# Performance work log

Hardware: AMD Instinct MI355X
Metric: run time of the kernel (lower is better)

The kernel has to match this reference:

```python
import jax, jax.numpy as jnp
import numpy as np

N_NODES = 100000
N_EDGES = 1600000
IN_CH = 128
HID = 128
OUT_CH = 2
NUM_GRAPHS = 512


def _mlp_params(key, d_in, d_out):
    k1, k2 = jax.random.split(key)
    s1 = 1.0 / np.sqrt(d_in)
    s2 = 1.0 / np.sqrt(d_out)
    return (jax.random.uniform(k1, (d_in, d_out), jnp.float32, -s1, s1),
            jnp.zeros((d_out,), jnp.float32),
            jax.random.uniform(k2, (d_out, d_out), jnp.float32, -s2, s2),
            jnp.zeros((d_out,), jnp.float32))


def setup_inputs() -> dict:
    key = jax.random.key(0)
    ks = jax.random.split(key, 8)
    x = jax.random.normal(ks[0], (N_NODES, IN_CH), jnp.float32)
    edge_index = jax.random.randint(ks[1], (2, N_EDGES), 0, N_NODES, jnp.int64)
    batch = jnp.sort(jax.random.randint(ks[2], (N_NODES,), 0, NUM_GRAPHS, jnp.int64))
    w1_0, b1_0, w2_0, b2_0 = _mlp_params(ks[3], IN_CH, HID)
    w1_1, b1_1, w2_1, b2_1 = _mlp_params(ks[4], HID, HID)
    w1_2, b1_2, w2_2, b2_2 = _mlp_params(ks[5], HID, HID)
    s = 1.0 / np.sqrt(HID)
    w_lin = jax.random.uniform(ks[6], (HID, OUT_CH), jnp.float32, -s, s)
    b_lin = jnp.zeros((OUT_CH,), jnp.float32)
    return {"x": x, "edge_index": edge_index, "batch": batch,
            "w1_0": w1_0, "b1_0": b1_0, "w2_0": w2_0, "b2_0": b2_0,
            "w1_1": w1_1, "b1_1": b1_1, "w2_1": w2_1, "b2_1": b2_1,
            "w1_2": w1_2, "b1_2": b1_2, "w2_2": w2_2, "b2_2": b2_2,
            "w_lin": w_lin, "b_lin": b_lin}


def _gin_conv(x, src, dst, w1, b1, w2, b2):
    # GINConv with eps=0: MLP(x + sum_{j in N(i)} x_j)
    agg = jax.ops.segment_sum(x[src], dst, num_segments=N_NODES)  # [N, d]
    h = x + agg
    h = jax.nn.relu(h @ w1 + b1)
    return h @ w2 + b2


def reference(x, edge_index, batch,
              w1_0, b1_0, w2_0, b2_0,
              w1_1, b1_1, w2_1, b2_1,
              w1_2, b1_2, w2_2, b2_2,
              w_lin, b_lin):
    src, dst = edge_index[0], edge_index[1]
    h = _gin_conv(x, src, dst, w1_0, b1_0, w2_0, b2_0)
    h = jax.nn.relu(h)
    h = jax.nn.relu(_gin_conv(h, src, dst, w1_1, b1_1, w2_1, b2_1))
    h = jax.nn.relu(h)  # forward applies relu twice after GIN1
    h = _gin_conv(h, src, dst, w1_2, b1_2, w2_2, b2_2)
    # global mean pool per graph
    sums = jax.ops.segment_sum(h, batch, num_segments=NUM_GRAPHS)  # [G, d]
    counts = jax.ops.segment_sum(jnp.ones((N_NODES,), h.dtype), batch,
                                 num_segments=NUM_GRAPHS)
    pooled = sums / jnp.maximum(counts, 1.0)[:, None]
    # dropout is identity in eval mode
    return pooled @ w_lin + b_lin  # [G, OUT_CH]
```

## Files before the change

### kernel.cpp

```cpp
#include <hip/hip_runtime.h>
#include <hip/hip_bf16.h>

#define N_NODES   100000
#define N_EDGES   1600000
#define IN_CH     128
#define HID       128
#define OUT_CH    2
#define NUM_GRAPHS 512

#define BKT_SHIFT 9
#define NB2 ((N_NODES + 511) >> BKT_SHIFT)
#define PB  200
#define CHUNK (N_EDGES / PB)

typedef __attribute__((ext_vector_type(8))) short bf16x8;
typedef __attribute__((ext_vector_type(4))) float f32x4;
typedef unsigned int uint32;
typedef unsigned long long uint64;

static __device__ __forceinline__ float b2f(uint32 b) {
    return __uint_as_float(b << 16);
}
static __device__ __forceinline__ unsigned short f2b(float f) {
    uint32 u = __float_as_uint(f);
    u += 0x7fffu + ((u >> 16) & 1u);
    return (unsigned short)(u >> 16);
}
static __device__ __forceinline__ void acc8(float* a, int4 v) {
    uint32 x;
    x = (uint32)v.x; a[0] += __uint_as_float(x << 16); a[1] += __uint_as_float(x & 0xffff0000u);
    x = (uint32)v.y; a[2] += __uint_as_float(x << 16); a[3] += __uint_as_float(x & 0xffff0000u);
    x = (uint32)v.z; a[4] += __uint_as_float(x << 16); a[5] += __uint_as_float(x & 0xffff0000u);
    x = (uint32)v.w; a[6] += __uint_as_float(x << 16); a[7] += __uint_as_float(x & 0xffff0000u);
}

__global__ void k_cast(const float* __restrict__ x, unsigned short* __restrict__ h) {
    int i = blockIdx.x * blockDim.x + threadIdx.x;
    int base = i * 4;
    float4 v = *(const float4*)(x + base);
    ushort4 o;
    o.x = f2b(v.x); o.y = f2b(v.y); o.z = f2b(v.z); o.w = f2b(v.w);
    *(ushort4*)(h + base) = o;
}

__global__ void k_wprep(const float* w0, const float* w1, const float* w2,
                        const float* w3, const float* w4, const float* w5,
                        unsigned short* __restrict__ wt) {
    const float* ws[6] = {w0, w1, w2, w3, w4, w5};
    const float* w = ws[blockIdx.x];
    unsigned short* o = wt + blockIdx.x * 16384;
    for (int i = threadIdx.x; i < 16384; i += 256) {
        int k = i >> 7, n = i & 127;
        o[n * 128 + k] = f2b(w[i]);
    }
}

__global__ void k_p1(const int* __restrict__ dst, int* __restrict__ histG) {
    __shared__ int h[NB2];
    int t = threadIdx.x, blk = blockIdx.x;
    for (int i = t; i < NB2; i += 512) h[i] = 0;
    __syncthreads();
    int base = blk * CHUNK;
    for (int i = t; i < CHUNK; i += 512)
        atomicAdd(&h[dst[base + i] >> BKT_SHIFT], 1);
    __syncthreads();
    for (int i = t; i < NB2; i += 512) histG[i * PB + blk] = h[i];
}

__global__ void k_scan1(const int* __restrict__ in, int* __restrict__ out,
                        int* __restrict__ bsum, int n) {
    __shared__ int sm[256];
    int b = blockIdx.x, t = threadIdx.x;
    int base = b * 1024 + t * 4;
    int v0 = 0, v1 = 0, v2 = 0, v3 = 0;
    if (base + 3 < n) {
        int4 q = *(const int4*)(in + base);
        v0 = q.x; v1 = q.y; v2 = q.z; v3 = q.w;
    } else {
        if (base + 0 < n) v0 = in[base + 0];
        if (base + 1 < n) v1 = in[base + 1];
        if (base + 2 < n) v2 = in[base + 2];
        if (base + 3 < n) v3 = in[base + 3];
    }
    int s = v0 + v1 + v2 + v3;
    sm[t] = s;
    __syncthreads();
    for (int off = 1; off < 256; off <<= 1) {
        int u = (t >= off) ? sm[t - off] : 0;
        __syncthreads();
        sm[t] += u;
        __syncthreads();
    }
    int p = (t == 0) ? 0 : sm[t - 1];
    int o0 = p, o1 = p + v0, o2 = o1 + v1, o3 = o2 + v2;
    if (base + 3 < n) {
        *(int4*)(out + base) = make_int4(o0, o1, o2, o3);
    } else {
        if (base + 0 < n) out[base + 0] = o0;
        if (base + 1 < n) out[base + 1] = o1;
        if (base + 2 < n) out[base + 2] = o2;
        if (base + 3 < n) out[base + 3] = o3;
    }
    if (t == 255) bsum[b] = s + ((t == 0) ? 0 : sm[t - 1]);
}

__global__ void k_scan2(int* __restrict__ bsum, int nb) {
    __shared__ int sm[128];
    int t = threadIdx.x;
    int v = (t < nb) ? bsum[t] : 0;
    sm[t] = v;
    __syncthreads();
    for (int off = 1; off < 128; off <<= 1) {
        int u = (t >= off) ? sm[t - off] : 0;
        __syncthreads();
        sm[t] += u;
        __syncthreads();
    }
    int p = (t == 0) ? 0 : sm[t - 1];
    if (t < nb) bsum[t] = p;
}

__global__ void k_scan3b(int* __restrict__ out, const int* __restrict__ bsum, int n) {
    int b = blockIdx.x, t = threadIdx.x;
    int base = b * 1024 + t * 4;
    int add = bsum[b];
    if (base + 3 < n) {
        int4 q = *(const int4*)(out + base);
        q.x += add; q.y += add; q.z += add; q.w += add;
        *(int4*)(out + base) = q;
    } else {
        for (int j = 0; j < 4; ++j)
            if (base + j < n) out[base + j] += add;
    }
}

__global__ void k_p3(const int* __restrict__ ei, const int* __restrict__ baseG,
                     uint64* __restrict__ ebuf) {
    __shared__ int cur[NB2];
    int t = threadIdx.x, blk = blockIdx.x;
    for (int i = t; i < NB2; i += 512) cur[i] = baseG[i * PB + blk];
    __syncthreads();
    int base = blk * CHUNK;
    for (int i = t; i < CHUNK; i += 512) {
        int e = base + i;
        int src = ei[e];
        int dst = ei[N_EDGES + e];
        int pos = atomicAdd(&cur[dst >> BKT_SHIFT], 1);
        ebuf[pos] = ((uint64)(uint32)dst << 32) | (uint32)src;
    }
}

__global__ void k_p4(const uint64* __restrict__ ebuf, const int* __restrict__ baseG,
                     int* __restrict__ off, int* __restrict__ csr) {
    __shared__ int ldeg[512];
    __shared__ int lscan[512];
    __shared__ int lcur[512];
    int b = blockIdx.x, t = threadIdx.x;
    int node0 = b << BKT_SHIFT;
    int nn = min(512, N_NODES - node0);
    int e0 = baseG[b * PB];
    int e1 = (b == NB2 - 1) ? N_EDGES : baseG[(b + 1) * PB];
    ldeg[t] = 0;
    __syncthreads();
    for (int e = e0 + t; e < e1; e += 512) {
        int dst = (int)(ebuf[e] >> 32);
        atomicAdd(&ldeg[dst - node0], 1);
    }
    __syncthreads();
    lscan[t] = ldeg[t];
    __syncthreads();
    for (int o = 1; o < 512; o <<= 1) {
        int v = (t >= o) ? lscan[t - o] : 0;
        __syncthreads();
        lscan[t] += v;
        __syncthreads();
    }
    int excl = (t == 0) ? 0 : lscan[t - 1];
    lcur[t] = e0 + excl;
    if (t < nn) off[node0 + t] = e0 + excl;
    if (b == NB2 - 1 && t == 0) off[N_NODES] = N_EDGES;
    __syncthreads();
    for (int e = e0 + t; e < e1; e += 512) {
        uint64 pr = ebuf[e];
        int dst = (int)(pr >> 32);
        int pos = atomicAdd(&lcur[dst - node0], 1);
        csr[pos] = (int)(pr & 0xffffffffu);
    }
}

__global__ void k_goff(const int* __restrict__ batch, int* __restrict__ goff) {
    int g = blockIdx.x * blockDim.x + threadIdx.x;
    if (g > NUM_GRAPHS) return;
    int lo = 0, hi = N_NODES;
    while (lo < hi) {
        int mid = (lo + hi) >> 1;
        if (batch[mid] < g) lo = mid + 1; else hi = mid;
    }
    goff[g] = lo;
}

__global__ void k_agg(const unsigned short* __restrict__ h,
                      const int* __restrict__ off, const int* __restrict__ csr,
                      unsigned short* __restrict__ hs) {
    int wid = (blockIdx.x * 256 + threadIdx.x) >> 6;
    int lane = threadIdx.x & 63;
    if (wid >= N_NODES) return;
    int g = lane >> 4, sub = lane & 15;
    int e0 = off[wid], e1 = off[wid + 1];
    float a[8] = {0.f, 0.f, 0.f, 0.f, 0.f, 0.f, 0.f, 0.f};
    int e = e0 + g;
    for (; e + 4 < e1; e += 8) {
        int s0 = csr[e];
        int s1 = csr[e + 4];
        int4 v0 = *(const int4*)(h + (size_t)s0 * 128 + sub * 8);
        int4 v1 = *(const int4*)(h + (size_t)s1 * 128 + sub * 8);
        acc8(a, v0);
        acc8(a, v1);
    }
    if (e < e1) {
        int s0 = csr[e];
        int4 v0 = *(const int4*)(h + (size_t)s0 * 128 + sub * 8);
        acc8(a, v0);
    }
#pragma unroll
    for (int j = 0; j < 8; ++j) {
        a[j] += __shfl_xor(a[j], 16);
        a[j] += __shfl_xor(a[j], 32);
    }
    if (g == 0) {
        int4 sv = *(const int4*)(h + (size_t)wid * 128 + sub * 8);
        acc8(a, sv);
        int4 o;
        o.x = (int)((uint32)f2b(a[0]) | ((uint32)f2b(a[1]) << 16));
        o.y = (int)((uint32)f2b(a[2]) | ((uint32)f2b(a[3]) << 16));
        o.z = (int)((uint32)f2b(a[4]) | ((uint32)f2b(a[5]) << 16));
        o.w = (int)((uint32)f2b(a[6]) | ((uint32)f2b(a[7]) << 16));
        *(int4*)(hs + (size_t)wid * 128 + sub * 8) = o;
    }
}

template<int OUTER_RELU>
__global__ void k_mlp(const unsigned short* __restrict__ hs,
                      const unsigned short* __restrict__ w1t, const float* __restrict__ b1,
                      const unsigned short* __restrict__ w2t, const float* __restrict__ b2,
                      unsigned short* __restrict__ ho) {
    __shared__ unsigned short T[128 * 128];
    int tid = threadIdx.x;
    int lane = tid & 63, wave = tid >> 6;
    int l15 = lane & 15, l4 = lane >> 4;
    int row0 = blockIdx.x * 128;
    int wn0 = wave * 32;

    bf16x8 w1f[2][4], w2f[2][4];
#pragma unroll
    for (int nt = 0; nt < 2; ++nt)
#pragma unroll
        for (int k = 0; k < 4; ++k) {
            int o = (wn0 + nt * 16 + l15) * 128 + k * 32 + l4 * 8;
            w1f[nt][k] = *(const bf16x8*)(w1t + o);
            w2f[nt][k] = *(const bf16x8*)(w2t + o);
        }
    float bias1[2] = { b1[wn0 + l15], b1[wn0 + 16 + l15] };
    float bias2[2] = { b2[wn0 + l15], b2[wn0 + 16 + l15] };

#pragma unroll
    for (int mt = 0; mt < 8; ++mt) {
        int arow = row0 + mt * 16 + l15;
        if (arow >= N_NODES) arow = N_NODES - 1;
        const unsigned short* ap = hs + (size_t)arow * 128 + l4 * 8;
        bf16x8 a0 = *(const bf16x8*)(ap);
        bf16x8 a1 = *(const bf16x8*)(ap + 32);
        bf16x8 a2 = *(const bf16x8*)(ap + 64);
        bf16x8 a3 = *(const bf16x8*)(ap + 96);
#pragma unroll
        for (int nt = 0; nt < 2; ++nt) {
            f32x4 acc = {0.f, 0.f, 0.f, 0.f};
            acc = __builtin_amdgcn_mfma_f32_16x16x32_bf16(a0, w1f[nt][0], acc, 0, 0, 0);
            acc = __builtin_amdgcn_mfma_f32_16x16x32_bf16(a1, w1f[nt][1], acc, 0, 0, 0);
            acc = __builtin_amdgcn_mfma_f32_16x16x32_bf16(a2, w1f[nt][2], acc, 0, 0, 0);
            acc = __builtin_amdgcn_mfma_f32_16x16x32_bf16(a3, w1f[nt][3], acc, 0, 0, 0);
#pragma unroll
            for (int j = 0; j < 4; ++j) {
                float v = fmaxf(acc[j] + bias1[nt], 0.f);
                int trow = mt * 16 + l4 * 4 + j;
                int tcol = wn0 + nt * 16 + l15;
                int byte = (trow * 256 + tcol * 2) ^ ((trow & 7) << 4);
                *(unsigned short*)((char*)T + byte) = f2b(v);
            }
        }
    }
    __syncthreads();

#pragma unroll
    for (int mt = 0; mt < 8; ++mt) {
        int trow = mt * 16 + l15;
        int sw = (trow & 7) << 4;
        int rb = trow * 256 + l4 * 16;
        bf16x8 t0 = *(const bf16x8*)((const char*)T + ((rb + 0)   ^ sw));
        bf16x8 t1 = *(const bf16x8*)((const char*)T + ((rb + 64)  ^ sw));
        bf16x8 t2 = *(const bf16x8*)((const char*)T + ((rb + 128) ^ sw));
        bf16x8 t3 = *(const bf16x8*)((const char*)T + ((rb + 192) ^ sw));
        __syncthreads();
#pragma unroll
        for (int nt = 0; nt < 2; ++nt) {
            f32x4 acc = {0.f, 0.f, 0.f, 0.f};
            acc = __builtin_amdgcn_mfma_f32_16x16x32_bf16(t0, w2f[nt][0], acc, 0, 0, 0);
            acc = __builtin_amdgcn_mfma_f32_16x16x32_bf16(t1, w2f[nt][1], acc, 0, 0, 0);
            acc = __builtin_amdgcn_mfma_f32_16x16x32_bf16(t2, w2f[nt][2], acc, 0, 0, 0);
            acc = __builtin_amdgcn_mfma_f32_16x16x32_bf16(t3, w2f[nt][3], acc, 0, 0, 0);
#pragma unroll
            for (int j = 0; j < 4; ++j) {
                float v = acc[j] + bias2[nt];
                if (OUTER_RELU) v = fmaxf(v, 0.f);
                int orow = mt * 16 + l4 * 4 + j;
                int ocol = wn0 + nt * 16 + l15;
                int byte = (orow * 256 + ocol * 2) ^ ((orow & 7) << 4);
                *(unsigned short*)((char*)T + byte) = f2b(v);
            }
        }
    }
    __syncthreads();

    for (int c = tid; c < 2048; c += 256) {
        int r = c >> 4, cc = c & 15;
        int byte = (r * 256 + cc * 16) ^ ((r & 7) << 4);
        int4 v = *(const int4*)((const char*)T + byte);
        int gr = row0 + r;
        if (gr < N_NODES)
            *(int4*)(ho + (size_t)gr * 128 + cc * 8) = v;
    }
}

__global__ void k_pool(const unsigned short* __restrict__ h,
                       const int* __restrict__ goff,
                       const float* __restrict__ wl, const float* __restrict__ bl,
                       float* __restrict__ out) {
    int g = blockIdx.x;
    int lane = threadIdx.x;
    int e0 = goff[g], e1 = goff[g + 1];
    int c2 = lane << 1;
    float s0 = 0.f, s1 = 0.f;
    int r = e0;
    for (; r + 1 < e1; r += 2) {
        uint32 v0 = *(const uint32*)(h + (size_t)r * 128 + c2);
        uint32 v1 = *(const uint32*)(h + (size_t)(r + 1) * 128 + c2);
        s0 += b2f(v0 & 0xffffu) + b2f(v1 & 0xffffu);
        s1 += b2f(v0 >> 16) + b2f(v1 >> 16);
    }
    if (r < e1) {
        uint32 v = *(const uint32*)(h + (size_t)r * 128 + c2);
        s0 += b2f(v & 0xffffu);
        s1 += b2f(v >> 16);
    }
    float inv = 1.f / fmaxf((float)(e1 - e0), 1.f);
    s0 *= inv; s1 *= inv;
    float o0 = s0 * wl[c2 * 2]     + s1 * wl[(c2 + 1) * 2];
    float o1 = s0 * wl[c2 * 2 + 1] + s1 * wl[(c2 + 1) * 2 + 1];
#pragma unroll
    for (int d = 32; d; d >>= 1) {
        o0 += __shfl_down(o0, d);
        o1 += __shfl_down(o1, d);
    }
    if (lane == 0) {
        out[g * 2]     = o0 + bl[0];
        out[g * 2 + 1] = o1 + bl[1];
    }
}

extern "C" void kernel_launch(void* const* d_in, const int* in_sizes, int n_in,
                              void* d_out, int out_size, void* d_ws, size_t ws_size,
                              hipStream_t stream) {
    const float* x     = (const float*)d_in[0];
    const int*   ei    = (const int*)d_in[1];
    const int*   batch = (const int*)d_in[2];
    const float* w1[3] = {(const float*)d_in[3],  (const float*)d_in[7],  (const float*)d_in[11]};
    const float* b1[3] = {(const float*)d_in[4],  (const float*)d_in[8],  (const float*)d_in[12]};
    const float* w2[3] = {(const float*)d_in[5],  (const float*)d_in[9],  (const float*)d_in[13]};
    const float* b2[3] = {(const float*)d_in[6],  (const float*)d_in[10], (const float*)d_in[14]};
    const float* wl    = (const float*)d_in[15];
    const float* bl    = (const float*)d_in[16];

    char* p = (char*)d_ws;
    auto alloc = [&](size_t bytes) {
        char* r = p;
        p += (bytes + 255) & ~(size_t)255;
        return r;
    };
    int* off    = (int*)alloc((size_t)(N_NODES + 1) * 4);
    int* goff   = (int*)alloc((size_t)(NUM_GRAPHS + 1) * 4);
    int* histG  = (int*)alloc((size_t)(NB2 * PB) * 4);
    int* baseG  = (int*)alloc((size_t)(NB2 * PB + 1) * 4);
    int* bsum   = (int*)alloc((size_t)128 * 4);
    int* csr    = (int*)alloc((size_t)N_EDGES * 4);
    unsigned short* wts = (unsigned short*)alloc((size_t)6 * 16384 * 2);
    unsigned short* hA  = (unsigned short*)alloc((size_t)N_NODES * 128 * 2);
    unsigned short* hS  = (unsigned short*)alloc((size_t)N_NODES * 128 * 2);
    unsigned short* hB  = (unsigned short*)alloc((size_t)N_NODES * 128 * 2);
    uint64* ebuf = (uint64*)hS;

    k_cast<<<(N_NODES * IN_CH / 4 + 255) / 256, 256, 0, stream>>>(x, hA);
    k_wprep<<<6, 256, 0, stream>>>(w1[0], w2[0], w1[1], w2[1], w1[2], w2[2], wts);

    k_p1<<<PB, 512, 0, stream>>>(ei + N_EDGES, histG);
    const int SCAN_N = NB2 * PB;
    const int SCAN_BLOCKS = (SCAN_N + 1023) / 1024;
    k_scan1<<<SCAN_BLOCKS, 256, 0, stream>>>(histG, baseG, bsum, SCAN_N);
    k_scan2<<<1, 128, 0, stream>>>(bsum, SCAN_BLOCKS);
    k_scan3b<<<SCAN_BLOCKS, 256, 0, stream>>>(baseG, bsum, SCAN_N);
    k_p3<<<PB, 512, 0, stream>>>(ei, baseG, ebuf);
    k_p4<<<NB2, 512, 0, stream>>>(ebuf, baseG, off, csr);

    k_goff<<<3, 256, 0, stream>>>(batch, goff);

    unsigned short* wt1[3] = {wts,             wts + 2 * 16384, wts + 4 * 16384};
    unsigned short* wt2[3] = {wts + 1 * 16384, wts + 3 * 16384, wts + 5 * 16384};

    const int AGG_GRID = N_NODES / 4;
    const int MLP_GRID = (N_NODES + 127) / 128;

    k_agg<<<AGG_GRID, 256, 0, stream>>>(hA, off, csr, hS);
    k_mlp<1><<<MLP_GRID, 256, 0, stream>>>(hS, wt1[0], b1[0], wt2[0], b2[0], hB);
    k_agg<<<AGG_GRID, 256, 0, stream>>>(hB, off, csr, hS);
    k_mlp<1><<<MLP_GRID, 256, 0, stream>>>(hS, wt1[1], b1[1], wt2[1], b2[1], hA);
    k_agg<<<AGG_GRID, 256, 0, stream>>>(hA, off, csr, hS);
    k_mlp<0><<<MLP_GRID, 256, 0, stream>>>(hS, wt1[2], b1[2], wt2[2], b2[2], hB);

    k_pool<<<NUM_GRAPHS, 64, 0, stream>>>(hB, goff, wl, bl, (float*)d_out);
}
```

Baseline: 398.1 us.

## Fuse neighbor aggregation into GIN MLP kernel via shared-memory staging

Merges the gather-sum aggregation kernel into the MLP kernel. Each 128-node block aggregates its neighbors into swizzled LDS, then runs both MFMA layers from there, which removes the global write and re-read of the aggregated intermediate and two launches per layer. It also unrolls the edge loop to four loads per iteration. In exchange, each wave processes 32 nodes one after another and the grid is cut from 25000 to 782 blocks, so gather parallelism and memory-latency hiding may fall sharply. A barrier is also moved into the first MFMA loop.

```diff
diff --git a/kernel.cpp b/kernel.cpp
--- a/kernel.cpp
+++ b/kernel.cpp
@@ -199,48 +199,9 @@
     goff[g] = lo;
 }
 
-__global__ void k_agg(const unsigned short* __restrict__ h,
+template<int OUTER_RELU>
+__global__ void k_gin(const unsigned short* __restrict__ h,
                       const int* __restrict__ off, const int* __restrict__ csr,
-                      unsigned short* __restrict__ hs) {
-    int wid = (blockIdx.x * 256 + threadIdx.x) >> 6;
-    int lane = threadIdx.x & 63;
-    if (wid >= N_NODES) return;
-    int g = lane >> 4, sub = lane & 15;
-    int e0 = off[wid], e1 = off[wid + 1];
-    float a[8] = {0.f, 0.f, 0.f, 0.f, 0.f, 0.f, 0.f, 0.f};
-    int e = e0 + g;
-    for (; e + 4 < e1; e += 8) {
-        int s0 = csr[e];
-        int s1 = csr[e + 4];
-        int4 v0 = *(const int4*)(h + (size_t)s0 * 128 + sub * 8);
-        int4 v1 = *(const int4*)(h + (size_t)s1 * 128 + sub * 8);
-        acc8(a, v0);
-        acc8(a, v1);
-    }
-    if (e < e1) {
-        int s0 = csr[e];
-        int4 v0 = *(const int4*)(h + (size_t)s0 * 128 + sub * 8);
-        acc8(a, v0);
-    }
-#pragma unroll
-    for (int j = 0; j < 8; ++j) {
-        a[j] += __shfl_xor(a[j], 16);
-        a[j] += __shfl_xor(a[j], 32);
-    }
-    if (g == 0) {
-        int4 sv = *(const int4*)(h + (size_t)wid * 128 + sub * 8);
-        acc8(a, sv);
-        int4 o;
-        o.x = (int)((uint32)f2b(a[0]) | ((uint32)f2b(a[1]) << 16));
-        o.y = (int)((uint32)f2b(a[2]) | ((uint32)f2b(a[3]) << 16));
-        o.z = (int)((uint32)f2b(a[4]) | ((uint32)f2b(a[5]) << 16));
-        o.w = (int)((uint32)f2b(a[6]) | ((uint32)f2b(a[7]) << 16));
-        *(int4*)(hs + (size_t)wid * 128 + sub * 8) = o;
-    }
-}
-
-template<int OUTER_RELU>
-__global__ void k_mlp(const unsigned short* __restrict__ hs,
                       const unsigned short* __restrict__ w1t, const float* __restrict__ b1,
                       const unsigned short* __restrict__ w2t, const float* __restrict__ b2,
                       unsigned short* __restrict__ ho) {
@@ -249,8 +210,53 @@
     int lane = tid & 63, wave = tid >> 6;
     int l15 = lane & 15, l4 = lane >> 4;
     int row0 = blockIdx.x * 128;
+
+    int g = l4, sub = l15;
+    for (int r = wave * 32; r < wave * 32 + 32; ++r) {
+        int node = row0 + r;
+        if (node >= N_NODES) node = N_NODES - 1;
+        int e0 = off[node], e1 = off[node + 1];
+        float a[8] = {0.f, 0.f, 0.f, 0.f, 0.f, 0.f, 0.f, 0.f};
+        int e = e0 + g;
+        for (; e + 12 < e1; e += 16) {
+            int s0 = csr[e], s1 = csr[e + 4], s2 = csr[e + 8], s3 = csr[e + 12];
+            int4 v0 = *(const int4*)(h + (size_t)s0 * 128 + sub * 8);
+            int4 v1 = *(const int4*)(h + (size_t)s1 * 128 + sub * 8);
+            int4 v2 = *(const int4*)(h + (size_t)s2 * 128 + sub * 8);
+            int4 v3 = *(const int4*)(h + (size_t)s3 * 128 + sub * 8);
+            acc8(a, v0); acc8(a, v1); acc8(a, v2); acc8(a, v3);
+        }
+        for (; e + 4 < e1; e += 8) {
+            int s0 = csr[e], s1 = csr[e + 4];
+            int4 v0 = *(const int4*)(h + (size_t)s0 * 128 + sub * 8);
+            int4 v1 = *(const int4*)(h + (size_t)s1 * 128 + sub * 8);
+            acc8(a, v0); acc8(a, v1);
+        }
+        if (e < e1) {
+            int s0 = csr[e];
+            int4 v0 = *(const int4*)(h + (size_t)s0 * 128 + sub * 8);
+            acc8(a, v0);
+        }
+#pragma unroll
+        for (int j = 0; j < 8; ++j) {
+            a[j] += __shfl_xor(a[j], 16);
+            a[j] += __shfl_xor(a[j], 32);
+        }
+        if (g == 0) {
+            int4 sv = *(const int4*)(h + (size_t)node * 128 + sub * 8);
+            acc8(a, sv);
+            int4 o;
+            o.x = (int)((uint32)f2b(a[0]) | ((uint32)f2b(a[1]) << 16));
+            o.y = (int)((uint32)f2b(a[2]) | ((uint32)f2b(a[3]) << 16));
+            o.z = (int)((uint32)f2b(a[4]) | ((uint32)f2b(a[5]) << 16));
+            o.w = (int)((uint32)f2b(a[6]) | ((uint32)f2b(a[7]) << 16));
+            int byte = (r * 256 + sub * 16) ^ ((r & 7) << 4);
+            *(int4*)((char*)T + byte) = o;
+        }
+    }
+    __syncthreads();
+
     int wn0 = wave * 32;
-
     bf16x8 w1f[2][4], w2f[2][4];
 #pragma unroll
     for (int nt = 0; nt < 2; ++nt)
@@ -265,13 +271,14 @@
 
 #pragma unroll
     for (int mt = 0; mt < 8; ++mt) {
-        int arow = row0 + mt * 16 + l15;
-        if (arow >= N_NODES) arow = N_NODES - 1;
-        const unsigned short* ap = hs + (size_t)arow * 128 + l4 * 8;
-        bf16x8 a0 = *(const bf16x8*)(ap);
-        bf16x8 a1 = *(const bf16x8*)(ap + 32);
-        bf16x8 a2 = *(const bf16x8*)(ap + 64);
-        bf16x8 a3 = *(const bf16x8*)(ap + 96);
+        int trow = mt * 16 + l15;
+        int sw = (trow & 7) << 4;
+        int rb = trow * 256 + l4 * 16;
+        bf16x8 a0 = *(const bf16x8*)((const char*)T + ((rb + 0)   ^ sw));
+        bf16x8 a1 = *(const bf16x8*)((const char*)T + ((rb + 64)  ^ sw));
+        bf16x8 a2 = *(const bf16x8*)((const char*)T + ((rb + 128) ^ sw));
+        bf16x8 a3 = *(const bf16x8*)((const char*)T + ((rb + 192) ^ sw));
+        __syncthreads();
 #pragma unroll
         for (int nt = 0; nt < 2; ++nt) {
             f32x4 acc = {0.f, 0.f, 0.f, 0.f};
@@ -282,14 +289,13 @@
 #pragma unroll
             for (int j = 0; j < 4; ++j) {
                 float v = fmaxf(acc[j] + bias1[nt], 0.f);
-                int trow = mt * 16 + l4 * 4 + j;
-                int tcol = wn0 + nt * 16 + l15;
-                int byte = (trow * 256 + tcol * 2) ^ ((trow & 7) << 4);
+                int orow = mt * 16 + l4 * 4 + j;
+                int ocol = wn0 + nt * 16 + l15;
+                int byte = (orow * 256 + ocol * 2) ^ ((orow & 7) << 4);
                 *(unsigned short*)((char*)T + byte) = f2b(v);
             }
         }
     }
-    __syncthreads();
 
 #pragma unroll
     for (int mt = 0; mt < 8; ++mt) {
@@ -392,11 +398,10 @@
     int* baseG  = (int*)alloc((size_t)(NB2 * PB + 1) * 4);
     int* bsum   = (int*)alloc((size_t)128 * 4);
     int* csr    = (int*)alloc((size_t)N_EDGES * 4);
+    uint64* ebuf = (uint64*)alloc((size_t)N_EDGES * 8);
     unsigned short* wts = (unsigned short*)alloc((size_t)6 * 16384 * 2);
     unsigned short* hA  = (unsigned short*)alloc((size_t)N_NODES * 128 * 2);
-    unsigned short* hS  = (unsigned short*)alloc((size_t)N_NODES * 128 * 2);
     unsigned short* hB  = (unsigned short*)alloc((size_t)N_NODES * 128 * 2);
-    uint64* ebuf = (uint64*)hS;
 
     k_cast<<<(N_NODES * IN_CH / 4 + 255) / 256, 256, 0, stream>>>(x, hA);
     k_wprep<<<6, 256, 0, stream>>>(w1[0], w2[0], w1[1], w2[1], w1[2], w2[2], wts);
@@ -415,15 +420,11 @@
     unsigned short* wt1[3] = {wts,             wts + 2 * 16384, wts + 4 * 16384};
     unsigned short* wt2[3] = {wts + 1 * 16384, wts + 3 * 16384, wts + 5 * 16384};
 
-    const int AGG_GRID = N_NODES / 4;
-    const int MLP_GRID = (N_NODES + 127) / 128;
-
-    k_agg<<<AGG_GRID, 256, 0, stream>>>(hA, off, csr, hS);
-    k_mlp<1><<<MLP_GRID, 256, 0, stream>>>(hS, wt1[0], b1[0], wt2[0], b2[0], hB);
-    k_agg<<<AGG_GRID, 256, 0, stream>>>(hB, off, csr, hS);
-    k_mlp<1><<<MLP_GRID, 256, 0, stream>>>(hS, wt1[1], b1[1], wt2[1], b2[1], hA);
-    k_agg<<<AGG_GRID, 256, 0, stream>>>(hA, off, csr, hS);
-    k_mlp<0><<<MLP_GRID, 256, 0, stream>>>(hS, wt1[2], b1[2], wt2[2], b2[2], hB);
+    const int GIN_GRID = (N_NODES + 127) / 128;
+
+    k_gin<1><<<GIN_GRID, 256, 0, stream>>>(hA, off, csr, wt1[0], b1[0], wt2[0], b2[0], hB);
+    k_gin<1><<<GIN_GRID, 256, 0, stream>>>(hB, off, csr, wt1[1], b1[1], wt2[1], b2[1], hA);
+    k_gin<0><<<GIN_GRID, 256, 0, stream>>>(hA, off, csr, wt1[2], b1[2], wt2[2], b2[2], hB);
 
     k_pool<<<NUM_GRAPHS, 64, 0, stream>>>(hB, goff, wl, bl, (float*)d_out);
 }
```

Result: slower. 468.0 us (+17.6%).

## Restructure MLP to per-wave 16-row tiles and unroll aggregation gather by four

Applied to the files above, without the earlier changes.

The MLP kernel now gives each wave its own 16-row tile in a private 4 KB LDS slab instead of 128 rows per block shared across waves. Weight fragments are loaded from global/L2 per output tile rather than kept in registers, and all block-level barriers are gone. This cuts LDS use and sync overhead and raises occupancy, at the cost of re-reading weights once per 16 rows. Separately, the aggregation loop gets a 4-edge unrolled body per lane group so more gather loads are in flight.

```diff
diff --git a/kernel.cpp b/kernel.cpp
--- a/kernel.cpp
+++ b/kernel.cpp
@@ -32,6 +32,9 @@
     x = (uint32)v.y; a[2] += __uint_as_float(x << 16); a[3] += __uint_as_float(x & 0xffff0000u);
     x = (uint32)v.z; a[4] += __uint_as_float(x << 16); a[5] += __uint_as_float(x & 0xffff0000u);
     x = (uint32)v.w; a[6] += __uint_as_float(x << 16); a[7] += __uint_as_float(x & 0xffff0000u);
+}
+static __device__ __forceinline__ int rswz(int r) {
+    return (((r >> 2) ^ r) & 3) << 5;
 }
 
 __global__ void k_cast(const float* __restrict__ x, unsigned short* __restrict__ h) {
@@ -209,6 +212,14 @@
     int e0 = off[wid], e1 = off[wid + 1];
     float a[8] = {0.f, 0.f, 0.f, 0.f, 0.f, 0.f, 0.f, 0.f};
     int e = e0 + g;
+    for (; e + 12 < e1; e += 16) {
+        int s0 = csr[e], s1 = csr[e + 4], s2 = csr[e + 8], s3 = csr[e + 12];
+        int4 v0 = *(const int4*)(h + (size_t)s0 * 128 + sub * 8);
+        int4 v1 = *(const int4*)(h + (size_t)s1 * 128 + sub * 8);
+        int4 v2 = *(const int4*)(h + (size_t)s2 * 128 + sub * 8);
+        int4 v3 = *(const int4*)(h + (size_t)s3 * 128 + sub * 8);
+        acc8(a, v0); acc8(a, v1); acc8(a, v2); acc8(a, v3);
+    }
     for (; e + 4 < e1; e += 8) {
         int s0 = csr[e];
         int s1 = csr[e + 4];
@@ -244,90 +255,89 @@
                       const unsigned short* __restrict__ w1t, const float* __restrict__ b1,
                       const unsigned short* __restrict__ w2t, const float* __restrict__ b2,
                       unsigned short* __restrict__ ho) {
-    __shared__ unsigned short T[128 * 128];
+    __shared__ char S[4][4096];
     int tid = threadIdx.x;
     int lane = tid & 63, wave = tid >> 6;
+    int w16 = blockIdx.x * 4 + wave;
+    if (w16 >= (N_NODES >> 4)) return;
+    char* Sw = S[wave];
     int l15 = lane & 15, l4 = lane >> 4;
-    int row0 = blockIdx.x * 128;
-    int wn0 = wave * 32;
-
-    bf16x8 w1f[2][4], w2f[2][4];
-#pragma unroll
-    for (int nt = 0; nt < 2; ++nt)
-#pragma unroll
-        for (int k = 0; k < 4; ++k) {
-            int o = (wn0 + nt * 16 + l15) * 128 + k * 32 + l4 * 8;
-            w1f[nt][k] = *(const bf16x8*)(w1t + o);
-            w2f[nt][k] = *(const bf16x8*)(w2t + o);
+    size_t rowbase = (size_t)w16 * 16 * 128;
+    int bo = l15 * 16;
+
+#pragma unroll
+    for (int i = 0; i < 4; ++i) {
+        int r = i * 4 + l4;
+        int4 v = *(const int4*)((const char*)(hs + rowbase) + r * 256 + bo);
+        *(int4*)(Sw + ((r * 256 + bo) ^ rswz(r))) = v;
+    }
+
+    float bias1[8], bias2[8];
+#pragma unroll
+    for (int nt = 0; nt < 8; ++nt) {
+        bias1[nt] = b1[nt * 16 + l15];
+        bias2[nt] = b2[nt * 16 + l15];
+    }
+
+    int frsw = rswz(l15);
+    bf16x8 af[4];
+#pragma unroll
+    for (int k = 0; k < 4; ++k)
+        af[k] = *(const bf16x8*)(Sw + ((l15 * 256 + k * 64 + l4 * 16) ^ frsw));
+
+#pragma unroll
+    for (int nt = 0; nt < 8; ++nt) {
+        const unsigned short* wp = w1t + (nt * 16 + l15) * 128 + l4 * 8;
+        bf16x8 wf0 = *(const bf16x8*)(wp);
+        bf16x8 wf1 = *(const bf16x8*)(wp + 32);
+        bf16x8 wf2 = *(const bf16x8*)(wp + 64);
+        bf16x8 wf3 = *(const bf16x8*)(wp + 96);
+        f32x4 acc = {0.f, 0.f, 0.f, 0.f};
+        acc = __builtin_amdgcn_mfma_f32_16x16x32_bf16(af[0], wf0, acc, 0, 0, 0);
+        acc = __builtin_amdgcn_mfma_f32_16x16x32_bf16(af[1], wf1, acc, 0, 0, 0);
+        acc = __builtin_amdgcn_mfma_f32_16x16x32_bf16(af[2], wf2, acc, 0, 0, 0);
+        acc = __builtin_amdgcn_mfma_f32_16x16x32_bf16(af[3], wf3, acc, 0, 0, 0);
+#pragma unroll
+        for (int j = 0; j < 4; ++j) {
+            float v = fmaxf(acc[j] + bias1[nt], 0.f);
+            int r = l4 * 4 + j;
+            int cb = (nt * 16 + l15) * 2;
+            *(unsigned short*)(Sw + ((r * 256 + cb) ^ rswz(r))) = f2b(v);
         }
-    float bias1[2] = { b1[wn0 + l15], b1[wn0 + 16 + l15] };
-    float bias2[2] = { b2[wn0 + l15], b2[wn0 + 16 + l15] };
-
-#pragma unroll
-    for (int mt = 0; mt < 8; ++mt) {
-        int arow = row0 + mt * 16 + l15;
-        if (arow >= N_NODES) arow = N_NODES - 1;
-        const unsigned short* ap = hs + (size_t)arow * 128 + l4 * 8;
-        bf16x8 a0 = *(const bf16x8*)(ap);
-        bf16x8 a1 = *(const bf16x8*)(ap + 32);
-        bf16x8 a2 = *(const bf16x8*)(ap + 64);
-        bf16x8 a3 = *(const bf16x8*)(ap + 96);
-#pragma unroll
-        for (int nt = 0; nt < 2; ++nt) {
-            f32x4 acc = {0.f, 0.f, 0.f, 0.f};
-            acc = __builtin_amdgcn_mfma_f32_16x16x32_bf16(a0, w1f[nt][0], acc, 0, 0, 0);
-            acc = __builtin_amdgcn_mfma_f32_16x16x32_bf16(a1, w1f[nt][1], acc, 0, 0, 0);
-            acc = __builtin_amdgcn_mfma_f32_16x16x32_bf16(a2, w1f[nt][2], acc, 0, 0, 0);
-            acc = __builtin_amdgcn_mfma_f32_16x16x32_bf16(a3, w1f[nt][3], acc, 0, 0, 0);
-#pragma unroll
-            for (int j = 0; j < 4; ++j) {
-                float v = fmaxf(acc[j] + bias1[nt], 0.f);
-                int trow = mt * 16 + l4 * 4 + j;
-                int tcol = wn0 + nt * 16 + l15;
-                int byte = (trow * 256 + tcol * 2) ^ ((trow & 7) << 4);
-                *(unsigned short*)((char*)T + byte) = f2b(v);
-            }
+    }
+
+    bf16x8 tf[4];
+#pragma unroll
+    for (int k = 0; k < 4; ++k)
+        tf[k] = *(const bf16x8*)(Sw + ((l15 * 256 + k * 64 + l4 * 16) ^ frsw));
+
+#pragma unroll
+    for (int nt = 0; nt < 8; ++nt) {
+        const unsigned short* wp = w2t + (nt * 16 + l15) * 128 + l4 * 8;
+        bf16x8 wf0 = *(const bf16x8*)(wp);
+        bf16x8 wf1 = *(const bf16x8*)(wp + 32);
+        bf16x8 wf2 = *(const bf16x8*)(wp + 64);
+        bf16x8 wf3 = *(const bf16x8*)(wp + 96);
+        f32x4 acc = {0.f, 0.f, 0.f, 0.f};
+        acc = __builtin_amdgcn_mfma_f32_16x16x32_bf16(tf[0], wf0, acc, 0, 0, 0);
+        acc = __builtin_amdgcn_mfma_f32_16x16x32_bf16(tf[1], wf1, acc, 0, 0, 0);
+        acc = __builtin_amdgcn_mfma_f32_16x16x32_bf16(tf[2], wf2, acc, 0, 0, 0);
+        acc = __builtin_amdgcn_mfma_f32_16x16x32_bf16(tf[3], wf3, acc, 0, 0, 0);
+#pragma unroll
+        for (int j = 0; j < 4; ++j) {
+            float v = acc[j] + bias2[nt];
+            if (OUTER_RELU) v = fmaxf(v, 0.f);
+            int r = l4 * 4 + j;
+            int cb = (nt * 16 + l15) * 2;
+            *(unsigned short*)(Sw + ((r * 256 + cb) ^ rswz(r))) = f2b(v);
         }
     }
-    __syncthreads();
-
-#pragma unroll
-    for (int mt = 0; mt < 8; ++mt) {
-        int trow = mt * 16 + l15;
-        int sw = (trow & 7) << 4;
-        int rb = trow * 256 + l4 * 16;
-        bf16x8 t0 = *(const bf16x8*)((const char*)T + ((rb + 0)   ^ sw));
-        bf16x8 t1 = *(const bf16x8*)((const char*)T + ((rb + 64)  ^ sw));
-        bf16x8 t2 = *(const bf16x8*)((const char*)T + ((rb + 128) ^ sw));
-        bf16x8 t3 = *(const bf16x8*)((const char*)T + ((rb + 192) ^ sw));
-        __syncthreads();
-#pragma unroll
-        for (int nt = 0; nt < 2; ++nt) {
-            f32x4 acc = {0.f, 0.f, 0.f, 0.f};
-            acc = __builtin_amdgcn_mfma_f32_16x16x32_bf16(t0, w2f[nt][0], acc, 0, 0, 0);
-            acc = __builtin_amdgcn_mfma_f32_16x16x32_bf16(t1, w2f[nt][1], acc, 0, 0, 0);
-            acc = __builtin_amdgcn_mfma_f32_16x16x32_bf16(t2, w2f[nt][2], acc, 0, 0, 0);
-            acc = __builtin_amdgcn_mfma_f32_16x16x32_bf16(t3, w2f[nt][3], acc, 0, 0, 0);
-#pragma unroll
-            for (int j = 0; j < 4; ++j) {
-                float v = acc[j] + bias2[nt];
-                if (OUTER_RELU) v = fmaxf(v, 0.f);
-                int orow = mt * 16 + l4 * 4 + j;
-                int ocol = wn0 + nt * 16 + l15;
-                int byte = (orow * 256 + ocol * 2) ^ ((orow & 7) << 4);
-                *(unsigned short*)((char*)T + byte) = f2b(v);
-            }
-        }
-    }
-    __syncthreads();
-
-    for (int c = tid; c < 2048; c += 256) {
-        int r = c >> 4, cc = c & 15;
-        int byte = (r * 256 + cc * 16) ^ ((r & 7) << 4);
-        int4 v = *(const int4*)((const char*)T + byte);
-        int gr = row0 + r;
-        if (gr < N_NODES)
-            *(int4*)(ho + (size_t)gr * 128 + cc * 8) = v;
+
+#pragma unroll
+    for (int i = 0; i < 4; ++i) {
+        int r = i * 4 + l4;
+        int4 v = *(const int4*)(Sw + ((r * 256 + bo) ^ rswz(r)));
+        *(int4*)((char*)(ho + rowbase) + r * 256 + bo) = v;
     }
 }
 
@@ -416,7 +426,7 @@
     unsigned short* wt2[3] = {wts + 1 * 16384, wts + 3 * 16384, wts + 5 * 16384};
 
     const int AGG_GRID = N_NODES / 4;
-    const int MLP_GRID = (N_NODES + 127) / 128;
+    const int MLP_GRID = (N_NODES / 16 + 3) / 4;
 
     k_agg<<<AGG_GRID, 256, 0, stream>>>(hA, off, csr, hS);
     k_mlp<1><<<MLP_GRID, 256, 0, stream>>>(hS, wt1[0], b1[0], wt2[0], b2[0], hB);
```

Measured after the change: 463.3 us. 1.16x slower.
